# Performance work log

Measured on AMD Instinct MI355X. Metric: run time of the kernel, lower is better.

Reference implementation:

```python
import jax, jax.numpy as jnp
import numpy as np

H = 8
DH = 64  # attention_head_size
HID = 512
NEG = -90000000000.0

def _lin(x, w, b):
    return x @ w + b

def _tfs(x):  # [N, HID] -> [H, N, DH]
    n = x.shape[0]
    return x.reshape(n, H, DH).transpose(1, 0, 2)

def _cross(q, ck, v, cv, mask, dw, db):
    # q: [H,N,DH], ck/cv: [H,M,DH], v: [H,N,DH], mask: [N,M]
    s = jnp.einsum('hnd,hmd->hnm', q, ck)
    s = s * mask[None, :, :] / jnp.sqrt(jnp.asarray(DH, s.dtype))
    s = jnp.where(s == 0.0, NEG, s)  # faithful zero->-inf hack
    p = jax.nn.softmax(s, axis=-1)
    ctx = v + jnp.einsum('hnm,hmd->hnd', p, cv)  # residual add of raw value
    n = ctx.shape[1]
    ctx = ctx.transpose(1, 0, 2).reshape(n, H * DH)
    return _lin(ctx, dw, db)

def setup_inputs() -> dict:
    key = jax.random.key(0)
    ks = jax.random.split(key, 24)
    N1, N2, D1 = 4096, 4096, 300
    d = {}
    d['h_head'] = jax.random.normal(ks[0], (N1, D1), jnp.float32)
    d['h_tail'] = jax.random.normal(ks[1], (N2, HID), jnp.float32)
    d['batch_head'] = jnp.sort(jax.random.randint(ks[2], (N1,), 0, 64))
    d['batch_tail'] = jnp.sort(jax.random.randint(ks[3], (N2,), 0, 64))
    def w(k, i, o):
        return jax.random.normal(k, (i, o), jnp.float32) / np.sqrt(i)
    d['map_w'] = w(ks[4], D1, HID); d['map_b'] = jnp.zeros((HID,), jnp.float32)
    names = ['q1', 'k1', 'v1', 'q2', 'k2', 'v2', 'd1', 'd2']
    for i, nm in enumerate(names):
        d[nm + '_w'] = w(ks[5 + i], HID, HID)
        d[nm + '_b'] = jnp.zeros((HID,), jnp.float32)
    return d

def reference(h_head, h_tail, batch_head, batch_tail,
              map_w, map_b,
              q1_w, q1_b, k1_w, k1_b, v1_w, v1_b,
              q2_w, q2_b, k2_w, k2_b, v2_w, v2_b,
              d1_w, d1_b, d2_w, d2_b):
    hh = _lin(h_head, map_w, map_b)  # n_dim1 != n_dim2 -> map
    q_h = _tfs(_lin(hh, q1_w, q1_b))
    k_h = _tfs(_lin(hh, k1_w, k1_b))
    v_h = _tfs(_lin(hh, v1_w, v1_b))
    q_t = _tfs(_lin(h_tail, q2_w, q2_b))
    k_t = _tfs(_lin(h_tail, k2_w, k2_b))
    v_t = _tfs(_lin(h_tail, v2_w, v2_b))
    mask = (batch_head[:, None] == batch_tail[None, :]).astype(jnp.float32)
    out_head = _cross(q_h, k_t, v_h, v_t, mask, d1_w, d1_b)
    out_tail = _cross(q_t, k_h, v_t, v_h, mask.T, d2_w, d2_b)
    return (out_head, out_tail)
```

## Files before the change

### kernel.cpp

```cpp
#include <hip/hip_runtime.h>
#include <hip/hip_bf16.h>
#include <math.h>


typedef __bf16 bf16x8 __attribute__((ext_vector_type(8)));
typedef float  f32x4  __attribute__((ext_vector_type(4)));

#define HID 512
#define NTOK 4096

#define AS1(p) ((const __attribute__((address_space(1))) void*)(p))
#define AS3(p) ((__attribute__((address_space(3))) void*)(p))

struct PrepArgs {
    const float* h_head; const float* h_tail;
    const int* bh; const int* bt;
    const float* map_w; const float* map_b;
    const float* qkvw[3]; const float* qkvb[3];
    const float* tsrc[8]; __bf16* tdst[8];
    __bf16* hh_bf; __bf16* ht_bf; __bf16* mapw_bf;
    float* fb;
    int* ranges;
};

__global__ __launch_bounds__(256) void fused_prep(PrepArgs pa) {
    const int q = blockIdx.x, z = blockIdx.z, tid = threadIdx.x;
    __shared__ __bf16 T[64][72];

    if (z == 0) {
        if (q == 0 && tid < 128) {
            int b = tid & 63;
            const int* arr = (tid < 64) ? pa.bh : pa.bt;
            int base = (tid < 64) ? 0 : 128;
            int lo = 0, hi = NTOK;
            while (lo < hi) { int mid = (lo + hi) >> 1; if (arr[mid] < b) lo = mid + 1; else hi = mid; }
            int start = lo;
            lo = 0; hi = NTOK;
            while (lo < hi) { int mid = (lo + hi) >> 1; if (arr[mid] <= b) lo = mid + 1; else hi = mid; }
            pa.ranges[base + b] = start;
            pa.ranges[base + 64 + b] = lo;
        }
        for (int idx = tid; idx < 8 * 40; idx += 256) {
            int r   = q * 8 + idx / 40;
            int col = (idx % 40) * 8;
            bf16x8 v;
            if (col + 8 <= 300) {
                float4 f0 = *(const float4*)&pa.h_head[(size_t)r * 300 + col];
                float4 f1 = *(const float4*)&pa.h_head[(size_t)r * 300 + col + 4];
                v[0]=(__bf16)f0.x; v[1]=(__bf16)f0.y; v[2]=(__bf16)f0.z; v[3]=(__bf16)f0.w;
                v[4]=(__bf16)f1.x; v[5]=(__bf16)f1.y; v[6]=(__bf16)f1.z; v[7]=(__bf16)f1.w;
            } else if (col < 300) {
                float4 f0 = *(const float4*)&pa.h_head[(size_t)r * 300 + col];
                v[0]=(__bf16)f0.x; v[1]=(__bf16)f0.y; v[2]=(__bf16)f0.z; v[3]=(__bf16)f0.w;
                v[4]=(__bf16)0.f; v[5]=(__bf16)0.f; v[6]=(__bf16)0.f; v[7]=(__bf16)0.f;
            } else {
                #pragma unroll
                for (int j = 0; j < 8; ++j) v[j] = (__bf16)0.f;
            }
            *(bf16x8*)&pa.hh_bf[(size_t)r * 320 + col] = v;
        }
    } else if (z == 1) {
        for (int idx = tid; idx < 8 * 64; idx += 256) {
            int r   = q * 8 + (idx >> 6);
            int col = (idx & 63) * 8;
            float4 f0 = *(const float4*)&pa.h_tail[(size_t)r * 512 + col];
            float4 f1 = *(const float4*)&pa.h_tail[(size_t)r * 512 + col + 4];
            bf16x8 v;
            v[0]=(__bf16)f0.x; v[1]=(__bf16)f0.y; v[2]=(__bf16)f0.z; v[3]=(__bf16)f0.w;
            v[4]=(__bf16)f1.x; v[5]=(__bf16)f1.y; v[6]=(__bf16)f1.z; v[7]=(__bf16)f1.w;
            *(bf16x8*)&pa.ht_bf[(size_t)r * 512 + col] = v;
        }
    } else if (z == 2) {
        if (q < 96) {
            int r   = q * 4 + (tid >> 6);
            int col = (tid & 63) * 8;
            bf16x8 v;
            if (r < 300) {
                float4 f0 = *(const float4*)&pa.map_w[(size_t)r * 512 + col];
                float4 f1 = *(const float4*)&pa.map_w[(size_t)r * 512 + col + 4];
                v[0]=(__bf16)f0.x; v[1]=(__bf16)f0.y; v[2]=(__bf16)f0.z; v[3]=(__bf16)f0.w;
                v[4]=(__bf16)f1.x; v[5]=(__bf16)f1.y; v[6]=(__bf16)f1.z; v[7]=(__bf16)f1.w;
            } else {
                #pragma unroll
                for (int j = 0; j < 8; ++j) v[j] = (__bf16)0.f;
            }
            *(bf16x8*)&pa.mapw_bf[(size_t)r * 512 + col] = v;
        } else if (q < 102) {
            int b2 = q - 96;
            int w  = b2 >> 1;
            int n  = ((b2 & 1) << 8) + tid;
            const float* W = pa.qkvw[w];
            float s = pa.qkvb[w][n];
            for (int j = 0; j < 512; ++j)
                s += pa.map_b[j] * W[(size_t)j * 512 + n];
            pa.fb[w * 512 + n] = s;
        }
    } else {
        if (q >= 64) return;
        const int jz = z - 3;
        const float* src = pa.tsrc[jz];
        __bf16* dst = pa.tdst[jz];
        const int tk = (q >> 3) * 64;
        const int tn = (q & 7) * 64;
        const int r0 = tid >> 4;
        const int c0 = (tid & 15) * 4;
        #pragma unroll
        for (int i = 0; i < 4; ++i) {
            float4 v = *(const float4*)&src[(size_t)(tk + r0 + i * 16) * 512 + tn + c0];
            T[r0 + i * 16][c0 + 0] = (__bf16)v.x;
            T[r0 + i * 16][c0 + 1] = (__bf16)v.y;
            T[r0 + i * 16][c0 + 2] = (__bf16)v.z;
            T[r0 + i * 16][c0 + 3] = (__bf16)v.w;
        }
        __syncthreads();
        const int n  = tid >> 2;
        const int kk = (tid & 3) * 16;
        bf16x8 o0, o1;
        #pragma unroll
        for (int j = 0; j < 8; ++j) { o0[j] = T[kk + j][n]; o1[j] = T[kk + 8 + j][n]; }
        __bf16* dp = dst + (size_t)(tn + n) * 512 + tk + kk;
        *(bf16x8*)dp       = o0;
        *(bf16x8*)(dp + 8) = o1;
    }
}

struct GemmJobs {
    const __bf16* A[6];
    const __bf16* W[6];
    const float*  bias[6];
    void*         C[6];
    int           Kp[6];
    int           ldC[6];
    int           Ncol[6];
};

template <typename TC>
__global__ __launch_bounds__(256) void gemm128(GemmJobs jobs) {
    __shared__ __align__(16) __bf16 As[2][4096];
    __shared__ __align__(16) __bf16 Bs[2][4096];

    const int z = blockIdx.z;
    const __bf16* A    = jobs.A[z];
    const __bf16* W    = jobs.W[z];
    const float*  bias = jobs.bias[z];
    TC*           C    = (TC*)jobs.C[z];
    const int     Kp   = jobs.Kp[z];

    const int tid  = threadIdx.x;
    const int wave = tid >> 6;
    const int lane = tid & 63;
    const int quad = lane >> 4;
    const int l16  = lane & 15;
    const int wy   = wave >> 1;
    const int wx   = wave & 1;
    const int rowBase = blockIdx.y * 128;
    const int colBase = blockIdx.x * 128;

    const int s_row = tid >> 2;
    const int s_kc  = ((tid & 3) ^ ((s_row >> 1) & 3)) * 8;

    const __bf16* gA = A + (size_t)(rowBase + s_row) * Kp + s_kc;
    const __bf16* gB = W + (size_t)(colBase + s_row) * Kp + s_kc;
    const int waveOff = wave * 512;

    f32x4 acc[4][4] = {};
    const int nk = Kp >> 5;

    __builtin_amdgcn_global_load_lds(AS1(gA),                   AS3(&As[0][waveOff]),        16, 0, 0);
    __builtin_amdgcn_global_load_lds(AS1(gA + (size_t)64 * Kp), AS3(&As[0][2048 + waveOff]), 16, 0, 0);
    __builtin_amdgcn_global_load_lds(AS1(gB),                   AS3(&Bs[0][waveOff]),        16, 0, 0);
    __builtin_amdgcn_global_load_lds(AS1(gB + (size_t)64 * Kp), AS3(&Bs[0][2048 + waveOff]), 16, 0, 0);

    for (int i = 0; i < nk; ++i) {
        const int cur = i & 1;
        __syncthreads();

        if (i + 1 < nk) {
            const int kt = (i + 1) * 32;
            const int nx = cur ^ 1;
            __builtin_amdgcn_global_load_lds(AS1(gA + kt),                   AS3(&As[nx][waveOff]),        16, 0, 0);
            __builtin_amdgcn_global_load_lds(AS1(gA + kt + (size_t)64 * Kp), AS3(&As[nx][2048 + waveOff]), 16, 0, 0);
            __builtin_amdgcn_global_load_lds(AS1(gB + kt),                   AS3(&Bs[nx][waveOff]),        16, 0, 0);
            __builtin_amdgcn_global_load_lds(AS1(gB + kt + (size_t)64 * Kp), AS3(&Bs[nx][2048 + waveOff]), 16, 0, 0);
        }

        bf16x8 ar[4], br[4];
        #pragma unroll
        for (int ii = 0; ii < 4; ++ii) {
            const int ra = wy * 64 + ii * 16 + l16;
            ar[ii] = *(const bf16x8*)&As[cur][ra * 32 + ((quad ^ ((ra >> 1) & 3)) << 3)];
        }
        #pragma unroll
        for (int jj = 0; jj < 4; ++jj) {
            const int rb = wx * 64 + jj * 16 + l16;
            br[jj] = *(const bf16x8*)&Bs[cur][rb * 32 + ((quad ^ ((rb >> 1) & 3)) << 3)];
        }
        #pragma unroll
        for (int ii = 0; ii < 4; ++ii)
            #pragma unroll
            for (int jj = 0; jj < 4; ++jj)
                acc[ii][jj] = __builtin_amdgcn_mfma_f32_16x16x32_bf16(ar[ii], br[jj], acc[ii][jj], 0, 0, 0);
    }

    const int ldC  = jobs.ldC[z];
    const int Ncol = jobs.Ncol[z];
    #pragma unroll
    for (int jj = 0; jj < 4; ++jj) {
        int col = colBase + wx * 64 + jj * 16 + l16;
        if (col < Ncol) {
            float bv = bias ? bias[col] : 0.f;
            #pragma unroll
            for (int ii = 0; ii < 4; ++ii) {
                #pragma unroll
                for (int r = 0; r < 4; ++r) {
                    int row = rowBase + wy * 64 + ii * 16 + quad * 4 + r;
                    C[(size_t)row * ldC + col] = (TC)(acc[ii][jj][r] + bv);
                }
            }
        }
    }
}

__global__ __launch_bounds__(256) void attn_mfma(
    const __bf16* __restrict__ Q0, const __bf16* __restrict__ K0,
    const __bf16* __restrict__ Vr0, const __bf16* __restrict__ Vc0,
    const __bf16* __restrict__ Q1, const __bf16* __restrict__ K1,
    const __bf16* __restrict__ Vr1, const __bf16* __restrict__ Vc1,
    const int* __restrict__ ranges,
    __bf16* __restrict__ O0, __bf16* __restrict__ O1,
    int Nq, int Nk)
{
    __shared__ __align__(16) __bf16 Qs[64][72];
    __shared__ __align__(16) __bf16 Ks[64][72];
    __shared__ __align__(16) __bf16 Vt[64][72];
    __shared__ __align__(16) __bf16 Ps[64][72];

    const int z = blockIdx.z;
    const __bf16* Q    = z ? Q1 : Q0;
    const __bf16* Kg   = z ? K1 : K0;
    const __bf16* Vres = z ? Vr1 : Vr0;
    const __bf16* Vctx = z ? Vc1 : Vc0;
    __bf16* Out        = z ? O1 : O0;
    const int* qstart  = z ? ranges + 128 : ranges;
    const int* qend    = z ? ranges + 192 : ranges + 64;
    const int* kstart  = z ? ranges       : ranges + 128;
    const int* kend    = z ? ranges + 64  : ranges + 192;

    const int h = blockIdx.x, b = blockIdx.y;
    const int qs = qstart[b], qe = qend[b];
    const int ts = kstart[b], te = kend[b];
    const int nq = qe - qs, nk = te - ts;
    if (nq <= 0) return;

    const int tid  = threadIdx.x;
    const int wave = tid >> 6;
    const int lane = tid & 63;
    const int quad = lane >> 4;
    const int l16  = lane & 15;
    const int srow = tid >> 2;
    const int scol = (tid & 3) * 16;

    if (nk <= 0) {
        float* meanv = (float*)Qs;
        if (tid < 64) {
            float s = 0.f;
            for (int m = 0; m < Nk; ++m)
                s += (float)Vctx[(size_t)m * HID + h * 64 + tid];
            meanv[tid] = s / (float)Nk;
        }
        __syncthreads();
        int d = tid & 63;
        for (int r = qs + (tid >> 6); r < qe; r += 4) {
            size_t off = (size_t)r * HID + h * 64 + d;
            Out[off] = (__bf16)((float)Vres[off] + meanv[d]);
        }
        return;
    }

    for (int qc = 0; qc < nq; qc += 64) {
        __syncthreads();
        {
            int qg = min(qs + qc + srow, Nq - 1);
            const __bf16* src = Q + (size_t)qg * HID + h * 64 + scol;
            *(bf16x8*)&Qs[srow][scol]     = *(const bf16x8*)src;
            *(bf16x8*)&Qs[srow][scol + 8] = *(const bf16x8*)(src + 8);
        }
        __syncthreads();
        bf16x8 aq0 = *(const bf16x8*)&Qs[wave * 16 + l16][quad * 8];
        bf16x8 aq1 = *(const bf16x8*)&Qs[wave * 16 + l16][32 + quad * 8];

        f32x4 O[4] = {};
        float Mx[4], L[4];
        #pragma unroll
        for (int r = 0; r < 4; ++r) { Mx[r] = -__builtin_inff(); L[r] = 0.f; }

        for (int kc = 0; kc < nk; kc += 64) {
            __syncthreads();
            {
                int kg = min(ts + kc + srow, Nk - 1);
                const __bf16* ksrc = Kg + (size_t)kg * HID + h * 64 + scol;
                *(bf16x8*)&Ks[srow][scol]     = *(const bf16x8*)ksrc;
                *(bf16x8*)&Ks[srow][scol + 8] = *(const bf16x8*)(ksrc + 8);
                const __bf16* vsrc = Vctx + (size_t)kg * HID + h * 64 + scol;
                bf16x8 v0 = *(const bf16x8*)vsrc;
                bf16x8 v1 = *(const bf16x8*)(vsrc + 8);
                #pragma unroll
                for (int j = 0; j < 8; ++j) {
                    Vt[scol + j][srow]     = v0[j];
                    Vt[scol + 8 + j][srow] = v1[j];
                }
            }
            __syncthreads();

            f32x4 S[4] = {};
            #pragma unroll
            for (int c = 0; c < 4; ++c) {
                bf16x8 bk0 = *(const bf16x8*)&Ks[c * 16 + l16][quad * 8];
                bf16x8 bk1 = *(const bf16x8*)&Ks[c * 16 + l16][32 + quad * 8];
                S[c] = __builtin_amdgcn_mfma_f32_16x16x32_bf16(aq0, bk0, S[c], 0, 0, 0);
                S[c] = __builtin_amdgcn_mfma_f32_16x16x32_bf16(aq1, bk1, S[c], 0, 0, 0);
            }

            #pragma unroll
            for (int c = 0; c < 4; ++c) {
                bool valid = (ts + kc + c * 16 + l16) < te;
                #pragma unroll
                for (int r = 0; r < 4; ++r)
                    S[c][r] = valid ? S[c][r] * 0.125f : -__builtin_inff();
            }

            float cm[4], ps[4], alpha[4];
            #pragma unroll
            for (int r = 0; r < 4; ++r) {
                float v = fmaxf(fmaxf(S[0][r], S[1][r]), fmaxf(S[2][r], S[3][r]));
                v = fmaxf(v, __shfl_xor(v, 1, 64));
                v = fmaxf(v, __shfl_xor(v, 2, 64));
                v = fmaxf(v, __shfl_xor(v, 4, 64));
                v = fmaxf(v, __shfl_xor(v, 8, 64));
                cm[r] = v;
            }
            #pragma unroll
            for (int r = 0; r < 4; ++r) {
                float nM = fmaxf(Mx[r], cm[r]);
                alpha[r] = __expf(Mx[r] - nM);
                Mx[r] = nM;
                ps[r] = 0.f;
            }
            #pragma unroll
            for (int c = 0; c < 4; ++c)
                #pragma unroll
                for (int r = 0; r < 4; ++r) {
                    float p = __expf(S[c][r] - Mx[r]);
                    S[c][r] = p;
                    ps[r] += p;
                }
            #pragma unroll
            for (int r = 0; r < 4; ++r) {
                float v = ps[r];
                v += __shfl_xor(v, 1, 64);
                v += __shfl_xor(v, 2, 64);
                v += __shfl_xor(v, 4, 64);
                v += __shfl_xor(v, 8, 64);
                L[r] = L[r] * alpha[r] + v;
            }
            #pragma unroll
            for (int c = 0; c < 4; ++c)
                #pragma unroll
                for (int r = 0; r < 4; ++r)
                    O[c][r] *= alpha[r];

            #pragma unroll
            for (int c = 0; c < 4; ++c)
                #pragma unroll
                for (int r = 0; r < 4; ++r)
                    Ps[wave * 16 + quad * 4 + r][c * 16 + l16] = (__bf16)S[c][r];
            __syncthreads();

            bf16x8 ap0 = *(const bf16x8*)&Ps[wave * 16 + l16][quad * 8];
            bf16x8 ap1 = *(const bf16x8*)&Ps[wave * 16 + l16][32 + quad * 8];
            #pragma unroll
            for (int c = 0; c < 4; ++c) {
                bf16x8 bv0 = *(const bf16x8*)&Vt[c * 16 + l16][quad * 8];
                bf16x8 bv1 = *(const bf16x8*)&Vt[c * 16 + l16][32 + quad * 8];
                O[c] = __builtin_amdgcn_mfma_f32_16x16x32_bf16(ap0, bv0, O[c], 0, 0, 0);
                O[c] = __builtin_amdgcn_mfma_f32_16x16x32_bf16(ap1, bv1, O[c], 0, 0, 0);
            }
        }

        #pragma unroll
        for (int c = 0; c < 4; ++c) {
            int d = h * 64 + c * 16 + l16;
            #pragma unroll
            for (int r = 0; r < 4; ++r) {
                int qrow = qs + qc + wave * 16 + quad * 4 + r;
                if (qrow < qe) {
                    size_t off = (size_t)qrow * HID + d;
                    Out[off] = (__bf16)((float)Vres[off] + O[c][r] / L[r]);
                }
            }
        }
    }
}

extern "C" void kernel_launch(void* const* d_in, const int* in_sizes, int n_in,
                              void* d_out, int out_size, void* d_ws, size_t ws_size,
                              hipStream_t stream) {
    (void)in_sizes; (void)n_in; (void)out_size; (void)ws_size;

    const float* h_head = (const float*)d_in[0];
    const float* h_tail = (const float*)d_in[1];
    const int* batch_head = (const int*)d_in[2];
    const int* batch_tail = (const int*)d_in[3];
    const float* map_w = (const float*)d_in[4];
    const float* map_b = (const float*)d_in[5];
    const float* q1_w = (const float*)d_in[6];
    const float* q1_b = (const float*)d_in[7];
    const float* k1_w = (const float*)d_in[8];
    const float* k1_b = (const float*)d_in[9];
    const float* v1_w = (const float*)d_in[10];
    const float* v1_b = (const float*)d_in[11];
    const float* q2_w = (const float*)d_in[12];
    const float* q2_b = (const float*)d_in[13];
    const float* k2_w = (const float*)d_in[14];
    const float* k2_b = (const float*)d_in[15];
    const float* v2_w = (const float*)d_in[16];
    const float* v2_b = (const float*)d_in[17];
    const float* d1_w = (const float*)d_in[18];
    const float* d1_b = (const float*)d_in[19];
    const float* d2_w = (const float*)d_in[20];
    const float* d2_b = (const float*)d_in[21];

    float* out = (float*)d_out;

    const size_t SZ = (size_t)NTOK * HID;
    char* ws = (char*)d_ws;
    int* ranges   = (int*)ws;
    __bf16* hh_bf = (__bf16*)(ws + 1024);
    __bf16* ht_bf = hh_bf + (size_t)NTOK * 320;
    __bf16* mapw_bf = ht_bf + SZ;
    __bf16* q1T  = mapw_bf + 384 * 512;
    __bf16* k1T  = q1T + 512 * 512;
    __bf16* v1T  = k1T + 512 * 512;
    __bf16* q2T  = v1T + 512 * 512;
    __bf16* k2T  = q2T + 512 * 512;
    __bf16* v2T  = k2T + 512 * 512;
    __bf16* d1T  = v2T + 512 * 512;
    __bf16* d2T  = d1T + 512 * 512;
    __bf16* FqT  = d2T + 512 * 512;
    __bf16* FkT  = FqT + 512 * 320;
    __bf16* FvT  = FkT + 512 * 320;
    __bf16* qh   = FvT + 512 * 320;
    __bf16* kh   = qh  + SZ;
    __bf16* vh   = kh  + SZ;
    __bf16* qt   = vh  + SZ;
    __bf16* kt   = qt  + SZ;
    __bf16* vt   = kt  + SZ;
    __bf16* ctxh = vt  + SZ;
    __bf16* ctxt = ctxh + SZ;
    float*  fb   = (float*)(ctxt + SZ);

    PrepArgs pa;
    pa.h_head = h_head; pa.h_tail = h_tail;
    pa.bh = batch_head; pa.bt = batch_tail;
    pa.map_w = map_w; pa.map_b = map_b;
    pa.qkvw[0] = q1_w; pa.qkvw[1] = k1_w; pa.qkvw[2] = v1_w;
    pa.qkvb[0] = q1_b; pa.qkvb[1] = k1_b; pa.qkvb[2] = v1_b;
    const float* wsrc[8] = {q1_w, k1_w, v1_w, q2_w, k2_w, v2_w, d1_w, d2_w};
    __bf16* wdst[8] = {q1T, k1T, v1T, q2T, k2T, v2T, d1T, d2T};
    for (int i = 0; i < 8; ++i) { pa.tsrc[i] = wsrc[i]; pa.tdst[i] = wdst[i]; }
    pa.hh_bf = hh_bf; pa.ht_bf = ht_bf; pa.mapw_bf = mapw_bf;
    pa.fb = fb; pa.ranges = ranges;
    fused_prep<<<dim3(512, 1, 11), dim3(256), 0, stream>>>(pa);

    {
        GemmJobs j;
        const __bf16* a3[3] = {q1T, k1T, v1T};
        __bf16* c3[3] = {FqT, FkT, FvT};
        for (int i = 0; i < 6; ++i) {
            int s = i < 3 ? i : 0;
            j.A[i] = a3[s]; j.W[i] = mapw_bf; j.bias[i] = nullptr;
            j.C[i] = c3[s]; j.Kp[i] = 512; j.ldC[i] = 320; j.Ncol[i] = 320;
        }
        gemm128<__bf16><<<dim3(3, 4, 3), dim3(256), 0, stream>>>(j);
    }

    {
        GemmJobs j;
        j.A[0] = hh_bf; j.W[0] = FqT; j.bias[0] = fb;        j.C[0] = qh; j.Kp[0] = 320;
        j.A[1] = hh_bf; j.W[1] = FkT; j.bias[1] = fb + 512;  j.C[1] = kh; j.Kp[1] = 320;
        j.A[2] = hh_bf; j.W[2] = FvT; j.bias[2] = fb + 1024; j.C[2] = vh; j.Kp[2] = 320;
        j.A[3] = ht_bf; j.W[3] = q2T; j.bias[3] = q2_b;      j.C[3] = qt; j.Kp[3] = 512;
        j.A[4] = ht_bf; j.W[4] = k2T; j.bias[4] = k2_b;      j.C[4] = kt; j.Kp[4] = 512;
        j.A[5] = ht_bf; j.W[5] = v2T; j.bias[5] = v2_b;      j.C[5] = vt; j.Kp[5] = 512;
        for (int i = 0; i < 6; ++i) { j.ldC[i] = HID; j.Ncol[i] = HID; }
        gemm128<__bf16><<<dim3(4, 32, 6), dim3(256), 0, stream>>>(j);
    }

    attn_mfma<<<dim3(8, 64, 2), dim3(256), 0, stream>>>(
        qh, kt, vh, vt,
        qt, kh, vt, vh,
        ranges, ctxh, ctxt, NTOK, NTOK);

    {
        GemmJobs j;
        for (int i = 0; i < 6; ++i) {
            int s = i < 2 ? i : 0;
            j.A[i] = s ? ctxt : ctxh;
            j.W[i] = s ? d2T : d1T;
            j.bias[i] = s ? d2_b : d1_b;
            j.C[i] = s ? (void*)(out + SZ) : (void*)out;
            j.Kp[i] = 512; j.ldC[i] = HID; j.Ncol[i] = HID;
        }
        gemm128<float><<<dim3(4, 32, 2), dim3(256), 0, stream>>>(j);
    }
}
```

Baseline: 193.8 us.

## Fold map-weight composition GEMM into prep kernel, drop separate launch

Moves the small GEMM that composes map_w with q1/k1/v1 weights (F = W^T·map_w^T) into the fused prep kernel as extra blocks. These blocks read the fp32 weights directly and convert them into LDS tiles, so the bf16 transposes of q1/k1/v1 and map_w are no longer produced. This removes one kernel launch and two intermediate workspace round-trips. The bias fold is also parallelised across four thread groups with a shared-memory reduction, and the GEMM epilogue is specialised to fixed ldC/Ncol. The cost is a longer critical path inside the prep launch, since these fold blocks run a full 16-step K loop without double buffering.

After: 198.3 us. 1.02x slower.

```diff
diff --git a/kernel.cpp b/kernel.cpp
--- a/kernel.cpp
+++ b/kernel.cpp
@@ -11,21 +11,121 @@
 
 #define AS1(p) ((const __attribute__((address_space(1))) void*)(p))
 #define AS3(p) ((__attribute__((address_space(3))) void*)(p))
+
+__device__ __forceinline__ void fold_tile(
+    const float* __restrict__ Wf,
+    const float* __restrict__ Mw,
+    __bf16* __restrict__ F,
+    int bx, int by, char* SMEM)
+{
+    __bf16* As = (__bf16*)SMEM;
+    __bf16* Bs = (__bf16*)(SMEM + 8192);
+
+    const int tid  = threadIdx.x;
+    const int wave = tid >> 6;
+    const int lane = tid & 63;
+    const int quad = lane >> 4;
+    const int l16  = lane & 15;
+    const int wy   = wave >> 1;
+    const int wx   = wave & 1;
+    const int rowBase = by * 128;
+    const int colBase = bx * 128;
+
+    const int s_row = tid >> 2;
+    const int s_gc  = (tid & 3) ^ ((s_row >> 1) & 3);
+    const int a_jj  = tid >> 3;
+    const int a_c16 = (tid & 7) * 16;
+    const int a_cp  = a_jj >> 3;
+    const int a_sub = a_jj & 7;
+
+    f32x4 acc[4][4] = {};
+
+    for (int i = 0; i < 16; ++i) {
+        const int j0 = i * 32;
+        __syncthreads();
+        #pragma unroll
+        for (int h = 0; h < 2; ++h) {
+            int r = s_row + h * 64;
+            int k = colBase + r;
+            bf16x8 v;
+            if (k < 300) {
+                const float* p = &Mw[(size_t)k * 512 + j0 + s_gc * 8];
+                float4 f0 = *(const float4*)p;
+                float4 f1 = *(const float4*)(p + 4);
+                v[0]=(__bf16)f0.x; v[1]=(__bf16)f0.y; v[2]=(__bf16)f0.z; v[3]=(__bf16)f0.w;
+                v[4]=(__bf16)f1.x; v[5]=(__bf16)f1.y; v[6]=(__bf16)f1.z; v[7]=(__bf16)f1.w;
+            } else {
+                #pragma unroll
+                for (int u = 0; u < 8; ++u) v[u] = (__bf16)0.f;
+            }
+            *(bf16x8*)&Bs[h * 2048 + tid * 8] = v;
+        }
+        {
+            const float* p = &Wf[(size_t)(j0 + a_jj) * 512 + rowBase + a_c16];
+            float4 f0 = *(const float4*)p;
+            float4 f1 = *(const float4*)(p + 4);
+            float4 f2 = *(const float4*)(p + 8);
+            float4 f3 = *(const float4*)(p + 12);
+            float vals[16] = {f0.x,f0.y,f0.z,f0.w, f1.x,f1.y,f1.z,f1.w,
+                              f2.x,f2.y,f2.z,f2.w, f3.x,f3.y,f3.z,f3.w};
+            #pragma unroll
+            for (int u = 0; u < 16; ++u) {
+                int r  = a_c16 + u;
+                int cp = a_cp ^ ((r >> 1) & 3);
+                As[r * 32 + cp * 8 + a_sub] = (__bf16)vals[u];
+            }
+        }
+        __syncthreads();
+
+        bf16x8 ar[4], br[4];
+        #pragma unroll
+        for (int ii = 0; ii < 4; ++ii) {
+            const int ra = wy * 64 + ii * 16 + l16;
+            ar[ii] = *(const bf16x8*)&As[ra * 32 + ((quad ^ ((ra >> 1) & 3)) << 3)];
+        }
+        #pragma unroll
+        for (int jj = 0; jj < 4; ++jj) {
+            const int rb = wx * 64 + jj * 16 + l16;
+            br[jj] = *(const bf16x8*)&Bs[rb * 32 + ((quad ^ ((rb >> 1) & 3)) << 3)];
+        }
+        #pragma unroll
+        for (int ii = 0; ii < 4; ++ii)
+            #pragma unroll
+            for (int jj = 0; jj < 4; ++jj)
+                acc[ii][jj] = __builtin_amdgcn_mfma_f32_16x16x32_bf16(ar[ii], br[jj], acc[ii][jj], 0, 0, 0);
+    }
+
+    #pragma unroll
+    for (int jj = 0; jj < 4; ++jj) {
+        int col = colBase + wx * 64 + jj * 16 + l16;
+        if (col < 320) {
+            #pragma unroll
+            for (int ii = 0; ii < 4; ++ii) {
+                #pragma unroll
+                for (int r = 0; r < 4; ++r) {
+                    int row = rowBase + wy * 64 + ii * 16 + quad * 4 + r;
+                    F[(size_t)row * 320 + col] = (__bf16)acc[ii][jj][r];
+                }
+            }
+        }
+    }
+}
 
 struct PrepArgs {
     const float* h_head; const float* h_tail;
     const int* bh; const int* bt;
     const float* map_w; const float* map_b;
     const float* qkvw[3]; const float* qkvb[3];
-    const float* tsrc[8]; __bf16* tdst[8];
-    __bf16* hh_bf; __bf16* ht_bf; __bf16* mapw_bf;
+    const float* tsrc[5]; __bf16* tdst[5];
+    __bf16* hh_bf; __bf16* ht_bf;
+    __bf16* F[3];
     float* fb;
     int* ranges;
 };
 
 __global__ __launch_bounds__(256) void fused_prep(PrepArgs pa) {
     const int q = blockIdx.x, z = blockIdx.z, tid = threadIdx.x;
-    __shared__ __bf16 T[64][72];
+    __shared__ __align__(16) char SMEM[32768];
 
     if (z == 0) {
         if (q == 0 && tid < 128) {
@@ -71,33 +171,32 @@
             *(bf16x8*)&pa.ht_bf[(size_t)r * 512 + col] = v;
         }
     } else if (z == 2) {
-        if (q < 96) {
-            int r   = q * 4 + (tid >> 6);
-            int col = (tid & 63) * 8;
-            bf16x8 v;
-            if (r < 300) {
-                float4 f0 = *(const float4*)&pa.map_w[(size_t)r * 512 + col];
-                float4 f1 = *(const float4*)&pa.map_w[(size_t)r * 512 + col + 4];
-                v[0]=(__bf16)f0.x; v[1]=(__bf16)f0.y; v[2]=(__bf16)f0.z; v[3]=(__bf16)f0.w;
-                v[4]=(__bf16)f1.x; v[5]=(__bf16)f1.y; v[6]=(__bf16)f1.z; v[7]=(__bf16)f1.w;
-            } else {
-                #pragma unroll
-                for (int j = 0; j < 8; ++j) v[j] = (__bf16)0.f;
-            }
-            *(bf16x8*)&pa.mapw_bf[(size_t)r * 512 + col] = v;
-        } else if (q < 102) {
-            int b2 = q - 96;
-            int w  = b2 >> 1;
-            int n  = ((b2 & 1) << 8) + tid;
-            const float* W = pa.qkvw[w];
-            float s = pa.qkvb[w][n];
-            for (int j = 0; j < 512; ++j)
-                s += pa.map_b[j] * W[(size_t)j * 512 + n];
-            pa.fb[w * 512 + n] = s;
-        }
+        if (q >= 24) return;
+        float* red = (float*)SMEM;
+        const int w  = q >> 3;
+        const int c8 = q & 7;
+        const int n  = c8 * 64 + (tid & 63);
+        const int jq = tid >> 6;
+        const float* W = pa.qkvw[w];
+        float s = 0.f;
+        for (int j = jq * 128; j < jq * 128 + 128; ++j)
+            s += pa.map_b[j] * W[(size_t)j * 512 + n];
+        red[tid] = s;
+        __syncthreads();
+        if (tid < 64) {
+            float r4 = red[tid] + red[64 + tid] + red[128 + tid] + red[192 + tid]
+                     + pa.qkvb[w][c8 * 64 + tid];
+            pa.fb[w * 512 + c8 * 64 + tid] = r4;
+        }
+    } else if (z == 3) {
+        if (q >= 36) return;
+        const int f = q / 12, t = q % 12;
+        fold_tile(pa.qkvw[f], pa.map_w, pa.F[f], t % 3, t / 3, SMEM);
     } else {
         if (q >= 64) return;
-        const int jz = z - 3;
+        typedef __bf16 trow[72];
+        trow* T = (trow*)SMEM;
+        const int jz = z - 4;
         const float* src = pa.tsrc[jz];
         __bf16* dst = pa.tdst[jz];
         const int tk = (q >> 3) * 64;
@@ -130,8 +229,6 @@
     const float*  bias[6];
     void*         C[6];
     int           Kp[6];
-    int           ldC[6];
-    int           Ncol[6];
 };
 
 template <typename TC>
@@ -202,20 +299,16 @@
                 acc[ii][jj] = __builtin_amdgcn_mfma_f32_16x16x32_bf16(ar[ii], br[jj], acc[ii][jj], 0, 0, 0);
     }
 
-    const int ldC  = jobs.ldC[z];
-    const int Ncol = jobs.Ncol[z];
     #pragma unroll
     for (int jj = 0; jj < 4; ++jj) {
         int col = colBase + wx * 64 + jj * 16 + l16;
-        if (col < Ncol) {
-            float bv = bias ? bias[col] : 0.f;
-            #pragma unroll
-            for (int ii = 0; ii < 4; ++ii) {
-                #pragma unroll
-                for (int r = 0; r < 4; ++r) {
-                    int row = rowBase + wy * 64 + ii * 16 + quad * 4 + r;
-                    C[(size_t)row * ldC + col] = (TC)(acc[ii][jj][r] + bv);
-                }
+        float bv = bias[col];
+        #pragma unroll
+        for (int ii = 0; ii < 4; ++ii) {
+            #pragma unroll
+            for (int r = 0; r < 4; ++r) {
+                int row = rowBase + wy * 64 + ii * 16 + quad * 4 + r;
+                C[(size_t)row * HID + col] = (TC)(acc[ii][jj][r] + bv);
             }
         }
     }
@@ -437,11 +530,7 @@
     int* ranges   = (int*)ws;
     __bf16* hh_bf = (__bf16*)(ws + 1024);
     __bf16* ht_bf = hh_bf + (size_t)NTOK * 320;
-    __bf16* mapw_bf = ht_bf + SZ;
-    __bf16* q1T  = mapw_bf + 384 * 512;
-    __bf16* k1T  = q1T + 512 * 512;
-    __bf16* v1T  = k1T + 512 * 512;
-    __bf16* q2T  = v1T + 512 * 512;
+    __bf16* q2T  = ht_bf + SZ;
     __bf16* k2T  = q2T + 512 * 512;
     __bf16* v2T  = k2T + 512 * 512;
     __bf16* d1T  = v2T + 512 * 512;
@@ -465,24 +554,13 @@
     pa.map_w = map_w; pa.map_b = map_b;
     pa.qkvw[0] = q1_w; pa.qkvw[1] = k1_w; pa.qkvw[2] = v1_w;
     pa.qkvb[0] = q1_b; pa.qkvb[1] = k1_b; pa.qkvb[2] = v1_b;
-    const float* wsrc[8] = {q1_w, k1_w, v1_w, q2_w, k2_w, v2_w, d1_w, d2_w};
-    __bf16* wdst[8] = {q1T, k1T, v1T, q2T, k2T, v2T, d1T, d2T};
-    for (int i = 0; i < 8; ++i) { pa.tsrc[i] = wsrc[i]; pa.tdst[i] = wdst[i]; }
-    pa.hh_bf = hh_bf; pa.ht_bf = ht_bf; pa.mapw_bf = mapw_bf;
+    const float* wsrc[5] = {q2_w, k2_w, v2_w, d1_w, d2_w};
+    __bf16* wdst[5] = {q2T, k2T, v2T, d1T, d2T};
+    for (int i = 0; i < 5; ++i) { pa.tsrc[i] = wsrc[i]; pa.tdst[i] = wdst[i]; }
+    pa.hh_bf = hh_bf; pa.ht_bf = ht_bf;
+    pa.F[0] = FqT; pa.F[1] = FkT; pa.F[2] = FvT;
     pa.fb = fb; pa.ranges = ranges;
-    fused_prep<<<dim3(512, 1, 11), dim3(256), 0, stream>>>(pa);
-
-    {
-        GemmJobs j;
-        const __bf16* a3[3] = {q1T, k1T, v1T};
-        __bf16* c3[3] = {FqT, FkT, FvT};
-        for (int i = 0; i < 6; ++i) {
-            int s = i < 3 ? i : 0;
-            j.A[i] = a3[s]; j.W[i] = mapw_bf; j.bias[i] = nullptr;
-            j.C[i] = c3[s]; j.Kp[i] = 512; j.ldC[i] = 320; j.Ncol[i] = 320;
-        }
-        gemm128<__bf16><<<dim3(3, 4, 3), dim3(256), 0, stream>>>(j);
-    }
+    fused_prep<<<dim3(512, 1, 9), dim3(256), 0, stream>>>(pa);
 
     {
         GemmJobs j;
@@ -492,7 +570,6 @@
         j.A[3] = ht_bf; j.W[3] = q2T; j.bias[3] = q2_b;      j.C[3] = qt; j.Kp[3] = 512;
         j.A[4] = ht_bf; j.W[4] = k2T; j.bias[4] = k2_b;      j.C[4] = kt; j.Kp[4] = 512;
         j.A[5] = ht_bf; j.W[5] = v2T; j.bias[5] = v2_b;      j.C[5] = vt; j.Kp[5] = 512;
-        for (int i = 0; i < 6; ++i) { j.ldC[i] = HID; j.Ncol[i] = HID; }
         gemm128<__bf16><<<dim3(4, 32, 6), dim3(256), 0, stream>>>(j);
     }
 
@@ -503,14 +580,12 @@
 
     {
         GemmJobs j;
-        for (int i = 0; i < 6; ++i) {
-            int s = i < 2 ? i : 0;
-            j.A[i] = s ? ctxt : ctxh;
-            j.W[i] = s ? d2T : d1T;
-            j.bias[i] = s ? d2_b : d1_b;
-            j.C[i] = s ? (void*)(out + SZ) : (void*)out;
-            j.Kp[i] = 512; j.ldC[i] = HID; j.Ncol[i] = HID;
-        }
+        j.A[0] = ctxh; j.W[0] = d1T; j.bias[0] = d1_b; j.C[0] = out;      j.Kp[0] = 512;
+        j.A[1] = ctxt; j.W[1] = d2T; j.bias[1] = d2_b; j.C[1] = out + SZ; j.Kp[1] = 512;
+        j.A[2] = ctxt; j.W[2] = d2T; j.bias[2] = d2_b; j.C[2] = out + SZ; j.Kp[2] = 512;
+        j.A[3] = ctxt; j.W[3] = d2T; j.bias[3] = d2_b; j.C[3] = out + SZ; j.Kp[3] = 512;
+        j.A[4] = ctxt; j.W[4] = d2T; j.bias[4] = d2_b; j.C[4] = out + SZ; j.Kp[4] = 512;
+        j.A[5] = ctxt; j.W[5] = d2T; j.bias[5] = d2_b; j.C[5] = out + SZ; j.Kp[5] = 512;
         gemm128<float><<<dim3(4, 32, 2), dim3(256), 0, stream>>>(j);
     }
 }
```
